# Optimization experiments

Hardware: AMD Instinct MI355X
Metric: run time of the kernel (lower is better)

Reference implementation:

```python
import jax, jax.numpy as jnp
import numpy as np

B, C, N, K, COUT = 4, 64, 8192, 16, 64
EPS = 1e-5  # BatchNorm1d default eps


def setup_inputs() -> dict:
    key = jax.random.key(0)
    k1, k2, k3 = jax.random.split(key, 3)
    x = jax.random.normal(k1, (B, C, N), dtype=jnp.float32)
    coords = jax.random.normal(k2, (B, 3, N), dtype=jnp.float32)
    # Linear(2C -> COUT) params
    W = jax.random.normal(k3, (2 * C, COUT), dtype=jnp.float32) * (1.0 / np.sqrt(2 * C))
    b = jnp.zeros((COUT,), dtype=jnp.float32)
    # BatchNorm1d affine params (train-mode batch stats, as in torch default)
    gamma = jnp.ones((COUT,), dtype=jnp.float32)
    beta = jnp.zeros((COUT,), dtype=jnp.float32)
    return {"x": x, "coords": coords, "W": W, "b": b, "gamma": gamma, "beta": beta}


def reference(x, coords, W, b, gamma, beta):
    k = min(K, max(N - 1, 1))
    # --- kNN in coordinate space (squared distances give same ordering as cdist) ---
    ct = jnp.swapaxes(coords, 1, 2)                      # (B, N, 3)
    sq = jnp.sum(ct * ct, axis=-1)                       # (B, N)
    d2 = sq[:, :, None] + sq[:, None, :] - 2.0 * jnp.einsum('bnd,bmd->bnm', ct, ct)
    _, idx = jax.lax.top_k(-d2, k + 1)                   # smallest k+1 distances
    idx = idx[:, :, 1:]                                  # drop self -> (B, N, k)
    # --- gather neighbor features ---
    xt = jnp.swapaxes(x, 1, 2)                           # (B, N, C)
    nb = jax.vmap(lambda f, i: f[i])(xt, idx)            # (B, N, k, C)
    center = jnp.broadcast_to(xt[:, :, None, :], nb.shape)
    edge = jnp.concatenate([center, nb - center], axis=-1)  # (B, N, k, 2C)
    # --- edge MLP: Linear -> BatchNorm1d (batch stats) -> ReLU ---
    h = jnp.einsum('bnkc,cd->bnkd', edge, W) + b         # (B, N, k, COUT)
    mean = jnp.mean(h, axis=(0, 1, 2))
    var = jnp.var(h, axis=(0, 1, 2))
    h = (h - mean) * jax.lax.rsqrt(var + EPS) * gamma + beta
    h = jax.nn.relu(h)
    # --- max-pool over k neighbors ---
    out = jnp.max(h, axis=2)                             # (B, N, COUT)
    return jnp.swapaxes(out, 1, 2)                       # (B, COUT, N)
```

## Files before the change

kernel.cpp:

```cpp
#include <hip/hip_runtime.h>


#define Bn 4
#define Cn 64
#define Nn 8192
#define Kn 16
#define CH 32
#define NSL 8

typedef unsigned long long ull;

__global__ __launch_bounds__(256) void transpose_kernel(const float* __restrict__ x,
                                                        const float* __restrict__ coords,
                                                        float* __restrict__ xt,
                                                        float4* __restrict__ cpack) {
  __shared__ float tile[64][65];
  int bid = blockIdx.x;
  int b = bid >> 7;
  int n0 = (bid & 127) << 6;
  int tx = threadIdx.x & 63;
  int ty = threadIdx.x >> 6;
  for (int c = ty; c < 64; c += 4)
    tile[tx][c] = x[((size_t)b * 64 + c) * Nn + n0 + tx];
  if (ty == 0) {
    int n = n0 + tx;
    const float* cb = coords + (size_t)b * 3 * Nn;
    float cx = cb[n], cy = cb[Nn + n], cz = cb[2 * Nn + n];
    float cs = __fadd_rn(__fadd_rn(__fmul_rn(cx, cx), __fmul_rn(cy, cy)),
                         __fmul_rn(cz, cz));
    cpack[(size_t)b * Nn + n] = make_float4(cx, cy, cz, cs);
  }
  __syncthreads();
  for (int r = ty; r < 64; r += 4)
    xt[((size_t)b * Nn + n0 + r) * 64 + tx] = tile[r][tx];
}


#define INSERT64(kv) do {                                     \
    ull _kk = (kv);                                           \
    bool _ci = _kk < ad[15];                                  \
    _Pragma("unroll")                                         \
    for (int _u = 15; _u >= 1; --_u) {                        \
      bool _cm = _kk < ad[_u - 1];                            \
      ull _nd = _cm ? ad[_u - 1] : _kk;                       \
      ad[_u] = _ci ? _nd : ad[_u];                            \
      _ci = _cm;                                              \
    }                                                         \
    ad[0] = _ci ? _kk : ad[0];                                \
    thr = ad[15];                                             \
  } while (0)

__global__ __launch_bounds__(512) void knn_kernel(const float4* __restrict__ cpack,
                                                  int* __restrict__ knn) {
  __shared__ ull mk[(NSL - 1) * 16][64];

  int bid = blockIdx.x;
  int b = bid >> 7;
  int q0 = (bid & 127) << 6;
  int tid = threadIdx.x;
  int q = tid & 63;
  int s = tid >> 6;
  int qg = q0 + q;

  const float4* cp = cpack + (size_t)b * Nn;
  float4 qc = cp[qg];
  float qs = qc.w;
  float qx2 = 2.f * qc.x, qy2 = 2.f * qc.y, qz2 = 2.f * qc.z;

  ull ad[16];
#pragma unroll
  for (int i = 0; i < 16; ++i) ad[i] = ~0ull;
  ull thr = ~0ull;
  unsigned thr_hi = 0xFFFFFFFFu;

  for (int c = 0; c < Nn / (NSL * CH); ++c) {
    int base = c * (NSL * CH) + s * CH;
    const float4* cpb = cp + base;
    unsigned mask = 0;
#pragma unroll 8
    for (int j = 0; j < CH; ++j) {
      float4 c4 = cpb[j];
      float dot2 = __fadd_rn(__fadd_rn(__fmul_rn(qx2, c4.x), __fmul_rn(qy2, c4.y)),
                             __fmul_rn(qz2, c4.z));
      float d2 = __fsub_rn(__fadd_rn(qs, c4.w), dot2);
      mask |= (__float_as_uint(d2) <= thr_hi) ? (1u << j) : 0u;
    }
    unsigned sj = (unsigned)(qg - base);
    if (sj < 32u) mask &= ~(1u << sj);
    while (__any(mask)) {
      if (mask) {
        int j = __ffs(mask) - 1;
        mask &= (mask - 1);
        float4 c4 = cpb[j];
        float dot2 = __fadd_rn(__fadd_rn(__fmul_rn(qx2, c4.x), __fmul_rn(qy2, c4.y)),
                               __fmul_rn(qz2, c4.z));
        float d2 = __fsub_rn(__fadd_rn(qs, c4.w), dot2);
        ull key = ((ull)__float_as_uint(d2) << 32) | (unsigned)(base + j);
        if (key < thr) INSERT64(key);
      }
    }
    thr_hi = (unsigned)(thr >> 32);
  }

  if (s > 0) {
#pragma unroll
    for (int i = 0; i < 16; ++i) mk[(s - 1) * 16 + i][q] = ad[i];
  }
  __syncthreads();
  if (s == 0) {
    for (int t = 0; t < (NSL - 1) * 16; ++t) {
      ull kk = mk[t][q];
      if (kk < thr) INSERT64(kk);
    }
    int* op = knn + (size_t)(b * Nn + qg) * 16;
#pragma unroll
    for (int i = 0; i < 16; ++i) op[i] = (int)(ad[i] & 0xFFFFFFFFull);
  }
}

__global__ __launch_bounds__(256) void edge_kernel(
    const float* __restrict__ xt, const int* __restrict__ knn,
    const float* __restrict__ W, const float* __restrict__ bias,
    float* __restrict__ mnb, float* __restrict__ mxb,
    float* __restrict__ ps1, float* __restrict__ ps2) {
  __shared__ float dlds[4][16][64];
  __shared__ float clds[4][64];
  __shared__ float r1[4][64], r2[4][64];

  int tid = threadIdx.x;
  int l = tid & 63;
  int w = tid >> 6;

  float w1[64], w2[64];
#pragma unroll
  for (int c = 0; c < 64; ++c) {
    w1[c] = W[c * 64 + l];
    w2[c] = W[(64 + c) * 64 + l];
  }
  float bl = bias[l];
  float s1 = 0.f, s2 = 0.f;

  int wid = blockIdx.x * 4 + w;
  int nw = gridDim.x * 4;
  for (int p = wid; p < Bn * Nn; p += nw) {
    int bb = p >> 13;
    const float* xb = xt + (size_t)bb * Nn * 64;
    float ctr = xt[(size_t)p * 64 + l];
    clds[w][l] = ctr;
    const int* ip = knn + (size_t)p * 16;
#pragma unroll
    for (int j = 0; j < 16; ++j) {
      int nj = ip[j];
      dlds[w][j][l] = xb[(size_t)nj * 64 + l] - ctr;
    }
    __syncthreads();

    float cc = bl;
#pragma unroll
    for (int c = 0; c < 64; ++c) cc = fmaf(clds[w][c], w1[c], cc);

    float mn = 3.0e38f, mx = -3.0e38f;
#pragma unroll
    for (int k = 0; k < 16; ++k) {
      float h = cc;
#pragma unroll
      for (int c = 0; c < 64; ++c) h = fmaf(dlds[w][k][c], w2[c], h);
      mn = fminf(mn, h);
      mx = fmaxf(mx, h);
      s1 += h;
      s2 = fmaf(h, h, s2);
    }
    mnb[(size_t)p * 64 + l] = mn;
    mxb[(size_t)p * 64 + l] = mx;
    __syncthreads();
  }

  r1[w][l] = s1; r2[w][l] = s2;
  __syncthreads();
  if (w == 0) {
    float a = r1[0][l] + r1[1][l] + r1[2][l] + r1[3][l];
    float c2 = r2[0][l] + r2[1][l] + r2[2][l] + r2[3][l];
    ps1[blockIdx.x * 64 + l] = a;
    ps2[blockIdx.x * 64 + l] = c2;
  }
}

__global__ __launch_bounds__(256) void stats_kernel(const float* __restrict__ ps1,
                                                    const float* __restrict__ ps2,
                                                    float* __restrict__ stats) {
  __shared__ float r1[4][64], r2[4][64];
  int c = threadIdx.x & 63, g = threadIdx.x >> 6;
  float a = 0.f, b2 = 0.f;
  for (int i = g; i < 512; i += 4) { a += ps1[i * 64 + c]; b2 += ps2[i * 64 + c]; }
  r1[g][c] = a; r2[g][c] = b2;
  __syncthreads();
  if (g == 0) {
    float s1 = r1[0][c] + r1[1][c] + r1[2][c] + r1[3][c];
    float s2 = r2[0][c] + r2[1][c] + r2[2][c] + r2[3][c];
    const float invM = 1.f / 524288.f;
    float mean = s1 * invM;
    float var = s2 * invM - mean * mean;
    stats[c] = mean;
    stats[64 + c] = var;
  }
}

__global__ __launch_bounds__(256) void final_kernel(
    const float* __restrict__ mnb, const float* __restrict__ mxb,
    const float* __restrict__ stats, const float* __restrict__ gamma,
    const float* __restrict__ beta, float* __restrict__ out) {
  __shared__ float tile[64][65];
  int bid = blockIdx.x;
  int b = bid >> 7;
  int n0 = (bid & 127) << 6;
  int tx = threadIdx.x & 63, ty = threadIdx.x >> 6;
  float mean = stats[tx], var = stats[64 + tx];
  float sc = gamma[tx] * rsqrtf(var + 1e-5f);
  float sh = fmaf(-mean, sc, beta[tx]);
  for (int r = ty; r < 64; r += 4) {
    size_t off = ((size_t)(b * Nn + n0 + r)) * 64 + tx;
    float lo = fmaf(mnb[off], sc, sh);
    float hi = fmaf(mxb[off], sc, sh);
    tile[tx][r] = fmaxf(fmaxf(hi, lo), 0.f);
  }
  __syncthreads();
  for (int r = ty; r < 64; r += 4)
    out[((size_t)b * 64 + r) * Nn + n0 + tx] = tile[r][tx];
}

extern "C" void kernel_launch(void* const* d_in, const int* in_sizes, int n_in,
                              void* d_out, int out_size, void* d_ws, size_t ws_size,
                              hipStream_t stream) {
  const float* x      = (const float*)d_in[0];
  const float* coords = (const float*)d_in[1];
  const float* W      = (const float*)d_in[2];
  const float* bias   = (const float*)d_in[3];
  const float* gamma  = (const float*)d_in[4];
  const float* beta   = (const float*)d_in[5];
  float* out = (float*)d_out;

  char* ws = (char*)d_ws;
  float*  xt    = (float*)ws;
  int*    knn   = (int*)(ws + 8388608);
  float*  mnb   = (float*)(ws + 10485760);
  float4* cpack = (float4*)(ws + 10485760);
  float*  mxb   = (float*)(ws + 18874368);
  float*  ps1   = (float*)(ws + 27262976);
  float*  ps2   = (float*)(ws + 27394048);
  float*  stats = (float*)(ws + 27525120);

  transpose_kernel<<<dim3(512), dim3(256), 0, stream>>>(x, coords, xt, cpack);
  knn_kernel<<<dim3(512), dim3(512), 0, stream>>>(cpack, knn);
  edge_kernel<<<dim3(512), dim3(256), 0, stream>>>(xt, knn, W, bias, mnb, mxb, ps1, ps2);
  stats_kernel<<<dim3(1), dim3(256), 0, stream>>>(ps1, ps2, stats);
  final_kernel<<<dim3(512), dim3(256), 0, stream>>>(mnb, mxb, stats, gamma, beta, out);
}
```

Before: 653.4 us.

## Stage candidate points in LDS and use unsorted replace-max kNN buffer

The kNN kernel now loads each tile of 512 candidate points into shared memory once per block, and all eight slices read from there instead of from global memory. The sorted 16-entry insertion network is replaced by an unsorted buffer: the current maximum is overwritten and a tree reduction finds the new maximum. Sentinel keys get distinct low bits so the equality-based replacement hits exactly one slot. This adds two block barriers per tile, and the output neighbour order is no longer sorted, which is harmless because the result is max-pooled over the neighbours.

```diff
diff --git a/kernel.cpp b/kernel.cpp
--- a/kernel.cpp
+++ b/kernel.cpp
@@ -5,7 +5,6 @@
 #define Cn 64
 #define Nn 8192
 #define Kn 16
-#define CH 32
 #define NSL 8
 
 typedef unsigned long long ull;
@@ -36,23 +35,32 @@
 }
 
 
-#define INSERT64(kv) do {                                     \
+#define RMAX(kv) do {                                         \
     ull _kk = (kv);                                           \
-    bool _ci = _kk < ad[15];                                  \
     _Pragma("unroll")                                         \
-    for (int _u = 15; _u >= 1; --_u) {                        \
-      bool _cm = _kk < ad[_u - 1];                            \
-      ull _nd = _cm ? ad[_u - 1] : _kk;                       \
-      ad[_u] = _ci ? _nd : ad[_u];                            \
-      _ci = _cm;                                              \
-    }                                                         \
-    ad[0] = _ci ? _kk : ad[0];                                \
-    thr = ad[15];                                             \
+    for (int _u = 0; _u < 16; ++_u)                           \
+      ad[_u] = (ad[_u] == thr) ? _kk : ad[_u];                \
+    ull _t0 = ad[0] > ad[1] ? ad[0] : ad[1];                  \
+    ull _t1 = ad[2] > ad[3] ? ad[2] : ad[3];                  \
+    ull _t2 = ad[4] > ad[5] ? ad[4] : ad[5];                  \
+    ull _t3 = ad[6] > ad[7] ? ad[6] : ad[7];                  \
+    ull _t4 = ad[8] > ad[9] ? ad[8] : ad[9];                  \
+    ull _t5 = ad[10] > ad[11] ? ad[10] : ad[11];              \
+    ull _t6 = ad[12] > ad[13] ? ad[12] : ad[13];              \
+    ull _t7 = ad[14] > ad[15] ? ad[14] : ad[15];              \
+    ull _u0 = _t0 > _t1 ? _t0 : _t1;                          \
+    ull _u1 = _t2 > _t3 ? _t2 : _t3;                          \
+    ull _u2 = _t4 > _t5 ? _t4 : _t5;                          \
+    ull _u3 = _t6 > _t7 ? _t6 : _t7;                          \
+    ull _v0 = _u0 > _u1 ? _u0 : _u1;                          \
+    ull _v1 = _u2 > _u3 ? _u2 : _u3;                          \
+    thr = _v0 > _v1 ? _v0 : _v1;                              \
   } while (0)
 
 __global__ __launch_bounds__(512) void knn_kernel(const float4* __restrict__ cpack,
                                                   int* __restrict__ knn) {
-  __shared__ ull mk[(NSL - 1) * 16][64];
+  __shared__ __align__(16) ull mk[(NSL - 1) * 16 * 64];
+  float4* stage = (float4*)mk;
 
   int bid = blockIdx.x;
   int b = bid >> 7;
@@ -69,48 +77,55 @@
 
   ull ad[16];
 #pragma unroll
-  for (int i = 0; i < 16; ++i) ad[i] = ~0ull;
-  ull thr = ~0ull;
+  for (int i = 0; i < 16; ++i) ad[i] = 0xFFFFFFFF00000000ull | (unsigned)i;
+  ull thr = 0xFFFFFFFF0000000Full;
   unsigned thr_hi = 0xFFFFFFFFu;
 
-  for (int c = 0; c < Nn / (NSL * CH); ++c) {
-    int base = c * (NSL * CH) + s * CH;
-    const float4* cpb = cp + base;
-    unsigned mask = 0;
+  for (int t = 0; t < Nn / 512; ++t) {
+    __syncthreads();
+    stage[tid] = cp[t * 512 + tid];
+    __syncthreads();
+#pragma unroll
+    for (int half = 0; half < 2; ++half) {
+      int loc = half * 256 + s * 32;
+      int base = t * 512 + loc;
+      unsigned mask = 0;
 #pragma unroll 8
-    for (int j = 0; j < CH; ++j) {
-      float4 c4 = cpb[j];
-      float dot2 = __fadd_rn(__fadd_rn(__fmul_rn(qx2, c4.x), __fmul_rn(qy2, c4.y)),
-                             __fmul_rn(qz2, c4.z));
-      float d2 = __fsub_rn(__fadd_rn(qs, c4.w), dot2);
-      mask |= (__float_as_uint(d2) <= thr_hi) ? (1u << j) : 0u;
-    }
-    unsigned sj = (unsigned)(qg - base);
-    if (sj < 32u) mask &= ~(1u << sj);
-    while (__any(mask)) {
-      if (mask) {
-        int j = __ffs(mask) - 1;
-        mask &= (mask - 1);
-        float4 c4 = cpb[j];
+      for (int j = 0; j < 32; ++j) {
+        float4 c4 = stage[loc + j];
         float dot2 = __fadd_rn(__fadd_rn(__fmul_rn(qx2, c4.x), __fmul_rn(qy2, c4.y)),
                                __fmul_rn(qz2, c4.z));
         float d2 = __fsub_rn(__fadd_rn(qs, c4.w), dot2);
-        ull key = ((ull)__float_as_uint(d2) << 32) | (unsigned)(base + j);
-        if (key < thr) INSERT64(key);
+        mask |= (__float_as_uint(d2) <= thr_hi) ? (1u << j) : 0u;
       }
-    }
-    thr_hi = (unsigned)(thr >> 32);
-  }
-
+      unsigned sj = (unsigned)(qg - base);
+      if (sj < 32u) mask &= ~(1u << sj);
+      while (__any(mask)) {
+        if (mask) {
+          int j = __ffs(mask) - 1;
+          mask &= (mask - 1);
+          float4 c4 = stage[loc + j];
+          float dot2 = __fadd_rn(__fadd_rn(__fmul_rn(qx2, c4.x), __fmul_rn(qy2, c4.y)),
+                                 __fmul_rn(qz2, c4.z));
+          float d2 = __fsub_rn(__fadd_rn(qs, c4.w), dot2);
+          ull key = ((ull)__float_as_uint(d2) << 32) | (unsigned)(base + j);
+          if (key < thr) RMAX(key);
+        }
+      }
+      thr_hi = (unsigned)(thr >> 32);
+    }
+  }
+
+  __syncthreads();
   if (s > 0) {
 #pragma unroll
-    for (int i = 0; i < 16; ++i) mk[(s - 1) * 16 + i][q] = ad[i];
+    for (int i = 0; i < 16; ++i) mk[(((s - 1) << 4) + i) * 64 + q] = ad[i];
   }
   __syncthreads();
   if (s == 0) {
     for (int t = 0; t < (NSL - 1) * 16; ++t) {
-      ull kk = mk[t][q];
-      if (kk < thr) INSERT64(kk);
+      ull kk = mk[t * 64 + q];
+      if (kk < thr) RMAX(kk);
     }
     int* op = knn + (size_t)(b * Nn + qg) * 16;
 #pragma unroll
```

After: 618.3 us. 5.4% less time.
